# Kernel tuning notes

Hardware: AMD Instinct MI355X
Metric: run time of the kernel (lower is better)

## Reference

```python
import jax, jax.numpy as jnp
import numpy as np

B, S, HID = 2, 2048, 2048
NH, NOPE, ROPE = 16, 128, 64
HD = NOPE + ROPE          # 192
VHD = 128
KVR, QR = 512, 1536
FFN = 5632
THETA = 10000.0
EPS = 1e-6


def rmsnorm(x, w, eps=EPS):
    xf = x.astype(jnp.float32)
    rms = jnp.sqrt(jnp.mean(xf * xf, axis=-1, keepdims=True) + eps)
    return (xf / rms).astype(x.dtype) * w


def apply_rope(x, cos, sin):
    # x: (..., rope_dim); half-split rotation convention
    half = x.shape[-1] // 2
    x1, x2 = x[..., :half], x[..., half:]
    return jnp.concatenate([x1 * cos - x2 * sin, x2 * cos + x1 * sin], axis=-1)


def rope_tables(seq_len, dim, theta=THETA):
    inv_freq = 1.0 / (theta ** (jnp.arange(0, dim, 2, dtype=jnp.float32) / dim))
    t = jnp.arange(seq_len, dtype=jnp.float32)
    freqs = jnp.outer(t, inv_freq)           # (S, dim/2)
    return jnp.cos(freqs), jnp.sin(freqs)


def setup_inputs():
    key = jax.random.key(0)
    ks = jax.random.split(key, 10)
    def w(k, shape, fan_in):
        return jax.random.normal(k, shape, dtype=jnp.float32) * (fan_in ** -0.5)
    return {
        'x': jax.random.normal(ks[0], (B, S, HID), dtype=jnp.float32),
        'attn_norm_w': jnp.ones((HID,), jnp.float32),
        'wq_down': w(ks[1], (HID, QR), HID),
        'wq_up': w(ks[2], (QR, NH * HD), QR),
        'wkv_down': w(ks[3], (HID, KVR + ROPE), HID),
        'kv_norm_w': jnp.ones((KVR,), jnp.float32),
        'wkv_up': w(ks[4], (KVR, NH * (NOPE + VHD)), KVR),
        'wout': w(ks[5], (NH * VHD, HID), NH * VHD),
        'ffn_norm_w': jnp.ones((HID,), jnp.float32),
        'w_gate': w(ks[6], (HID, FFN), HID),
        'w_up': w(ks[7], (HID, FFN), HID),
        'w_down': w(ks[8], (FFN, HID), FFN),
    }


def reference(x, attn_norm_w, wq_down, wq_up, wkv_down, kv_norm_w, wkv_up, wout,
              ffn_norm_w, w_gate, w_up, w_down):
    scale = 1.0 / np.sqrt(HD)
    # --- attention sub-block ---
    h = rmsnorm(x, attn_norm_w)
    q = (h @ wq_down) @ wq_up                       # (B,S,NH*HD)
    q = q.reshape(B, S, NH, HD)
    q_nope, q_rope = q[..., :NOPE], q[..., NOPE:]
    kv_full = h @ wkv_down                          # (B,S,KVR+ROPE)
    kv_c, k_rope = kv_full[..., :KVR], kv_full[..., KVR:]
    kv_c = rmsnorm(kv_c, kv_norm_w)
    kv_exp = (kv_c @ wkv_up).reshape(B, S, NH, NOPE + VHD)
    k_nope, v = kv_exp[..., :NOPE], kv_exp[..., NOPE:]

    cos, sin = rope_tables(S, ROPE)                 # (S, ROPE/2)
    cos4, sin4 = cos[None, :, None, :], sin[None, :, None, :]
    q_rope = apply_rope(q_rope, cos4, sin4)         # (B,S,NH,ROPE)
    k_rope = apply_rope(k_rope[:, :, None, :], cos4, sin4)  # (B,S,1,ROPE)
    k_rope = jnp.broadcast_to(k_rope, (B, S, NH, ROPE))

    q_full = jnp.concatenate([q_nope, q_rope], axis=-1)     # (B,S,NH,HD)
    k = jnp.concatenate([k_nope, k_rope], axis=-1)          # (B,S,NH,HD)

    scores = jnp.einsum('bqhd,bkhd->bhqk', q_full, k) * scale
    causal = jnp.tril(jnp.ones((S, S), dtype=bool))
    scores = jnp.where(causal[None, None], scores, jnp.finfo(scores.dtype).min)
    probs = jax.nn.softmax(scores, axis=-1)
    attn = jnp.einsum('bhqk,bkhd->bqhd', probs, v).reshape(B, S, NH * VHD)
    x = x + attn @ wout

    # --- SwiGLU MLP sub-block ---
    h2 = rmsnorm(x, ffn_norm_w)
    ffn = (jax.nn.silu(h2 @ w_gate) * (h2 @ w_up)) @ w_down
    return x + ffn
```

## Files before the change

### kernel.cpp

```cpp
#include <hip/hip_runtime.h>
#include <hip/hip_bf16.h>


using bf16x8 = __attribute__((ext_vector_type(8))) short;
using f32x4  = __attribute__((ext_vector_type(4))) float;

#define GLOBAL_AS __attribute__((address_space(1)))
#define LDS_AS    __attribute__((address_space(3)))
#define MFMA16(a, b, c) __builtin_amdgcn_mfma_f32_16x16x32_bf16((a), (b), (c), 0, 0, 0)

static constexpr int Sc = 2048;

__device__ __forceinline__ void gload16(const void* g, void* l) {
  __builtin_amdgcn_global_load_lds((const GLOBAL_AS unsigned int*)g,
                                   (LDS_AS unsigned int*)l, 16, 0, 0);
}
__device__ __forceinline__ float bf2f(unsigned short u) {
  union { float f; unsigned int i; } x; x.i = ((unsigned int)u) << 16; return x.f;
}
__device__ __forceinline__ unsigned short f2bf(float f) {
  union { float f; unsigned int i; } x; x.f = f;
  unsigned int i = x.i;
  return (unsigned short)((i + 0x7fffu + ((i >> 16) & 1u)) >> 16);
}
__device__ __forceinline__ int swz4(int r) { return ((r >> 2) & 3) ^ (r & 3); }

__global__ void fill_k(float* out, float v, int n) {
  int i = blockIdx.x * 256 + threadIdx.x;
  if (i < n) out[i] = v;
}

__global__ __launch_bounds__(256) void wtrans(const float* __restrict__ W,
                                              unsigned short* __restrict__ WT,
                                              int K, int N) {
  __shared__ float t[64][65];
  const int n0 = blockIdx.x * 64, k0 = blockIdx.y * 64;
  const int tx = threadIdx.x & 15, ty = threadIdx.x >> 4;
#pragma unroll
  for (int i = 0; i < 4; ++i) {
    int k = k0 + ty + i * 16;
    const float4 v = *(const float4*)(W + (size_t)k * N + n0 + tx * 4);
    t[ty + i * 16][tx * 4 + 0] = v.x;
    t[ty + i * 16][tx * 4 + 1] = v.y;
    t[ty + i * 16][tx * 4 + 2] = v.z;
    t[ty + i * 16][tx * 4 + 3] = v.w;
  }
  __syncthreads();
  const int kx = threadIdx.x & 7, ny = threadIdx.x >> 3;
#pragma unroll
  for (int i = 0; i < 2; ++i) {
    int nl = ny + i * 32;
    unsigned short u[8];
#pragma unroll
    for (int j = 0; j < 8; ++j) u[j] = f2bf(t[kx * 8 + j][nl]);
    *(uint4*)(WT + (size_t)(n0 + nl) * K + k0 + kx * 8) = *(uint4*)u;
  }
}

__global__ void rope_tab(float* __restrict__ cosT, float* __restrict__ sinT) {
  int i = blockIdx.x * 256 + threadIdx.x;
  if (i >= Sc * 32) return;
  int s = i >> 5, j = i & 31;
  float inv = powf(10000.0f, -(float)j / 32.0f);
  float a = (float)s * inv;
  cosT[i] = cosf(a);
  sinT[i] = sinf(a);
}

__global__ __launch_bounds__(256) void rmsnorm_k(const float* __restrict__ in,
                                                 const float* __restrict__ w,
                                                 unsigned short* __restrict__ out,
                                                 int D, int istride, int ostride) {
  const int row = blockIdx.x;
  const float* x = in + (size_t)row * istride;
  float ss = 0.f;
  for (int c = threadIdx.x * 4; c < D; c += 1024) {
    const float4 v = *(const float4*)(x + c);
    ss += v.x * v.x + v.y * v.y + v.z * v.z + v.w * v.w;
  }
#pragma unroll
  for (int off = 1; off < 64; off <<= 1) ss += __shfl_xor(ss, off);
  __shared__ float part[4];
  if ((threadIdx.x & 63) == 0) part[threadIdx.x >> 6] = ss;
  __syncthreads();
  float tot = part[0] + part[1] + part[2] + part[3];
  float r = rsqrtf(tot / (float)D + 1e-6f);
  for (int c = threadIdx.x * 4; c < D; c += 1024) {
    const float4 v = *(const float4*)(x + c);
    ushort4 o;
    o.x = f2bf(v.x * r * w[c + 0]);
    o.y = f2bf(v.y * r * w[c + 1]);
    o.z = f2bf(v.z * r * w[c + 2]);
    o.w = f2bf(v.w * r * w[c + 3]);
    *(ushort4*)(out + (size_t)row * ostride + c) = o;
  }
}

enum { EPI_BF16 = 0, EPI_F32 = 1, EPI_ADDF32 = 2, EPI_SILU = 3 };

template <int EPI>
__global__ __launch_bounds__(256) void gemm_sb1(const unsigned short* __restrict__ A,
                                                const unsigned short* __restrict__ BT,
                                                void* __restrict__ Cp,
                                                const float* __restrict__ resid,
                                                const unsigned short* __restrict__ other,
                                                int M, int N, int K) {
  __shared__ unsigned short ldsA[128 * 64];
  __shared__ unsigned short ldsB[128 * 64];
  const int tid = threadIdx.x;
  const int w = tid >> 6, lane = tid & 63;
  const int rl = lane & 15, gh = lane >> 4;
  const int wm = (w >> 1) * 64, wn = (w & 1) * 64;

  const int nwg = gridDim.x;
  const int orig = blockIdx.x;
  const int qq = nwg >> 3, rr = nwg & 7;
  const int xcd = orig & 7, lidx = orig >> 3;
  const int fswz = (xcd < rr ? xcd * (qq + 1) : rr * (qq + 1) + (xcd - rr) * qq) + lidx;
  const int MT = M >> 7;
  const int m0 = (fswz % MT) * 128;
  const int n0 = (fswz / MT) * 128;

  const unsigned short* sA[4];
  const unsigned short* sB[4];
#pragma unroll
  for (int i = 0; i < 4; ++i) {
    int G = i * 256 + tid, r = G >> 3, sl = (G & 7) ^ (r & 7);
    sA[i] = A + (size_t)(m0 + r) * K + sl * 8;
    sB[i] = BT + (size_t)(n0 + r) * K + sl * 8;
  }
  auto STAGE = [&](int kt) {
    const int ko = kt * 64;
#pragma unroll
    for (int i = 0; i < 4; ++i) {
      gload16(sA[i] + ko, &ldsA[(i * 256 + w * 64) * 8]);
      gload16(sB[i] + ko, &ldsB[(i * 256 + w * 64) * 8]);
    }
  };

  int aoff[4], boff[4];
#pragma unroll
  for (int i = 0; i < 4; ++i) {
    aoff[i] = (wm + i * 16 + rl) * 64;
    boff[i] = (wn + i * 16 + rl) * 64;
  }

  f32x4 acc[4][4] = {};
  const int nk = K >> 6;

  STAGE(0);
  asm volatile("s_waitcnt vmcnt(0)" ::: "memory");
  __builtin_amdgcn_s_barrier();

  for (int kt = 0; kt < nk; ++kt) {
    bf16x8 a[4][2], b[4][2];
#pragma unroll
    for (int i = 0; i < 4; ++i)
#pragma unroll
      for (int ks = 0; ks < 2; ++ks) {
        const int ra = wm + i * 16 + rl;
        a[i][ks] = *(const bf16x8*)&ldsA[aoff[i] + ((((ks << 2) + gh)) ^ (ra & 7)) * 8];
        const int rb = wn + i * 16 + rl;
        b[i][ks] = *(const bf16x8*)&ldsB[boff[i] + ((((ks << 2) + gh)) ^ (rb & 7)) * 8];
      }
    asm volatile("s_waitcnt lgkmcnt(0)" ::: "memory");
    __builtin_amdgcn_sched_barrier(0);
    __builtin_amdgcn_s_setprio(1);
#pragma unroll
    for (int i = 0; i < 4; ++i)
#pragma unroll
      for (int j = 0; j < 4; ++j) acc[i][j] = MFMA16(a[i][0], b[j][0], acc[i][j]);
    __builtin_amdgcn_s_setprio(0);
    __builtin_amdgcn_sched_barrier(0);
    __builtin_amdgcn_s_barrier();
    STAGE((kt + 1 < nk) ? kt + 1 : nk - 1);
    __builtin_amdgcn_sched_barrier(0);
    __builtin_amdgcn_s_setprio(1);
#pragma unroll
    for (int i = 0; i < 4; ++i)
#pragma unroll
      for (int j = 0; j < 4; ++j) acc[i][j] = MFMA16(a[i][1], b[j][1], acc[i][j]);
    __builtin_amdgcn_s_setprio(0);
    __builtin_amdgcn_sched_barrier(0);
    asm volatile("s_waitcnt vmcnt(0)" ::: "memory");
    __builtin_amdgcn_s_barrier();
  }

#pragma unroll
  for (int i = 0; i < 4; ++i) {
#pragma unroll
    for (int j = 0; j < 4; ++j) {
#pragma unroll
      for (int rg = 0; rg < 4; ++rg) {
        const int row = m0 + wm + i * 16 + gh * 4 + rg;
        const int col = n0 + wn + j * 16 + rl;
        const size_t idx = (size_t)row * N + col;
        const float v = acc[i][j][rg];
        if constexpr (EPI == EPI_BF16) {
          ((unsigned short*)Cp)[idx] = f2bf(v);
        } else if constexpr (EPI == EPI_F32) {
          ((float*)Cp)[idx] = v;
        } else if constexpr (EPI == EPI_ADDF32) {
          ((float*)Cp)[idx] = v + resid[idx];
        } else {
          float gv = bf2f(other[idx]);
          float sg = gv / (1.f + __expf(-gv));
          ((unsigned short*)Cp)[idx] = f2bf(sg * v);
        }
      }
    }
  }
}

template <int EPI>
__global__ __launch_bounds__(256) void gemm_bt(const unsigned short* __restrict__ A,
                                               const unsigned short* __restrict__ BT,
                                               void* __restrict__ Cp,
                                               const float* __restrict__ resid,
                                               const unsigned short* __restrict__ other,
                                               int M, int N, int K) {
  __shared__ unsigned short ldsA[2][128 * 32];
  __shared__ unsigned short ldsB[2][128 * 32];
  const int tid = threadIdx.x;
  const int w = tid >> 6, lane = tid & 63;
  const int nwg = gridDim.x;
  const int orig = blockIdx.x;
  const int qq = nwg >> 3, rr = nwg & 7;
  const int xcd = orig & 7, lidx = orig >> 3;
  const int fswz = (xcd < rr ? xcd * (qq + 1) : rr * (qq + 1) + (xcd - rr) * qq) + lidx;
  const int m0 = (fswz & 31) * 128;
  const int n0 = (fswz >> 5) * 128;

  const int wm = (w >> 1) * 64, wn = (w & 1) * 64;
  const int rl = lane & 15, gsel = lane >> 4;

  const int p0 = w * 64 + lane;
  const int p1 = p0 + 256;
  const int r0 = p0 >> 2, r1 = p1 >> 2;
  const int g0 = (p0 & 3) ^ swz4(r0), g1 = (p1 & 3) ^ swz4(r1);
  const unsigned short* gA0 = A + (size_t)(m0 + r0) * K + g0 * 8;
  const unsigned short* gA1 = A + (size_t)(m0 + r1) * K + g1 * 8;
  const unsigned short* gB0 = BT + (size_t)(n0 + r0) * K + g0 * 8;
  const unsigned short* gB1 = BT + (size_t)(n0 + r1) * K + g1 * 8;
  const int dA0 = (w * 64) * 8, dA1 = dA0 + 2048;

  int aoff[4], boff[4];
#pragma unroll
  for (int i = 0; i < 4; ++i) {
    int ra = wm + i * 16 + rl;
    aoff[i] = ra * 32 + (gsel ^ swz4(ra)) * 8;
    int rb = wn + i * 16 + rl;
    boff[i] = rb * 32 + (gsel ^ swz4(rb)) * 8;
  }

  auto STAGE = [&](int kt, int p) {
    const int ko = kt * 32;
    gload16(gA0 + ko, &ldsA[p][dA0]);
    gload16(gA1 + ko, &ldsA[p][dA1]);
    gload16(gB0 + ko, &ldsB[p][dA0]);
    gload16(gB1 + ko, &ldsB[p][dA1]);
  };

  f32x4 acc[4][4] = {};
  const int nk = K >> 5;

  STAGE(0, 0);
  STAGE(1, 1);
  for (int kt = 0; kt < nk; ++kt) {
    asm volatile("s_waitcnt vmcnt(4)" ::: "memory");
    __builtin_amdgcn_s_barrier();
    __builtin_amdgcn_sched_barrier(0);
    const unsigned short* lA = &ldsA[kt & 1][0];
    const unsigned short* lB = &ldsB[kt & 1][0];
    bf16x8 a[4], b[4];
#pragma unroll
    for (int i = 0; i < 4; ++i) a[i] = *(const bf16x8*)&lA[aoff[i]];
#pragma unroll
    for (int i = 0; i < 4; ++i) b[i] = *(const bf16x8*)&lB[boff[i]];
    __builtin_amdgcn_s_setprio(1);
#pragma unroll
    for (int i = 0; i < 4; ++i)
#pragma unroll
      for (int j = 0; j < 4; ++j) acc[i][j] = MFMA16(a[i], b[j], acc[i][j]);
    __builtin_amdgcn_s_setprio(0);
    __builtin_amdgcn_sched_barrier(0);
    __builtin_amdgcn_s_barrier();
    const int nxt = (kt + 2 < nk) ? kt + 2 : nk - 1;
    STAGE(nxt, kt & 1);
  }

#pragma unroll
  for (int i = 0; i < 4; ++i) {
#pragma unroll
    for (int j = 0; j < 4; ++j) {
#pragma unroll
      for (int rg = 0; rg < 4; ++rg) {
        const int row = m0 + wm + i * 16 + gsel * 4 + rg;
        const int col = n0 + wn + j * 16 + rl;
        const size_t idx = (size_t)row * N + col;
        const float v = acc[i][j][rg];
        if constexpr (EPI == EPI_BF16) {
          ((unsigned short*)Cp)[idx] = f2bf(v);
        } else if constexpr (EPI == EPI_F32) {
          ((float*)Cp)[idx] = v;
        } else if constexpr (EPI == EPI_ADDF32) {
          ((float*)Cp)[idx] = v + resid[idx];
        } else {
          float gv = bf2f(other[idx]);
          float sg = gv / (1.f + __expf(-gv));
          ((unsigned short*)Cp)[idx] = f2bf(sg * v);
        }
      }
    }
  }
}

__global__ __launch_bounds__(256) void repack_q(const unsigned short* __restrict__ q,
                                                const float* __restrict__ cosT,
                                                const float* __restrict__ sinT,
                                                unsigned short* __restrict__ Qc) {
  const int row = blockIdx.x;
  const int b = row >> 11, s = row & 2047;
  const float scale = 0.07216878364870322f;
  const unsigned short* qr = q + (size_t)row * 3072;
  for (int i = threadIdx.x; i < 3072; i += 256) {
    int h = i / 192, d = i - h * 192;
    float v;
    if (d < 128) {
      v = bf2f(qr[h * 192 + d]);
    } else {
      int j = d - 128;
      int jj = j & 31;
      float x1 = bf2f(qr[h * 192 + 128 + jj]);
      float x2 = bf2f(qr[h * 192 + 160 + jj]);
      float c = cosT[s * 32 + jj], sn = sinT[s * 32 + jj];
      v = (j < 32) ? (x1 * c - x2 * sn) : (x2 * c + x1 * sn);
    }
    Qc[((size_t)(b * 16 + h) * Sc + s) * 192 + d] = f2bf(v * scale);
  }
}

__global__ __launch_bounds__(256) void repack_kv(const unsigned short* __restrict__ kvex,
                                                 const float* __restrict__ kvf,
                                                 const float* __restrict__ cosT,
                                                 const float* __restrict__ sinT,
                                                 unsigned short* __restrict__ Kc,
                                                 unsigned short* __restrict__ VT) {
  __shared__ unsigned short vt_lds[32][136];
  const int bid = blockIdx.x;
  const int st = bid & 63;
  const int h = (bid >> 6) & 15;
  const int b = bid >> 10;
  const int s0 = st * 32;
  const int tid = threadIdx.x;
  const size_t KcBase = (size_t)(b * 16 + h) * Sc;
  for (int i = tid; i < 32 * 32; i += 256) {
    int r = i >> 5, g = i & 31;
    uint4 vdat = *(const uint4*)(kvex + (size_t)(b * Sc + s0 + r) * 4096 + h * 256 + g * 8);
    if (g < 16) {
      *(uint4*)(Kc + (KcBase + s0 + r) * 192 + g * 8) = vdat;
    } else {
      *(uint4*)(&vt_lds[r][(g - 16) * 8]) = vdat;
    }
  }
  for (int i = tid; i < 32 * 64; i += 256) {
    int r = i >> 6, d = i & 63;
    int s = s0 + r;
    int jj = d & 31;
    const float* kvrow = kvf + (size_t)(b * Sc + s) * 640;
    float x1 = kvrow[512 + jj], x2 = kvrow[544 + jj];
    float c = cosT[s * 32 + jj], sn = sinT[s * 32 + jj];
    float v = (d < 32) ? (x1 * c - x2 * sn) : (x2 * c + x1 * sn);
    Kc[(KcBase + s) * 192 + 128 + d] = f2bf(v);
  }
  __syncthreads();
  const int f = tid >> 1, sh = (tid & 1) * 16;
  unsigned int vals[8];
#pragma unroll
  for (int k2 = 0; k2 < 8; ++k2) {
    unsigned int lo = vt_lds[sh + 2 * k2][f];
    unsigned int hi = vt_lds[sh + 2 * k2 + 1][f];
    vals[k2] = lo | (hi << 16);
  }
  unsigned short* dst = VT + ((size_t)(b * 16 + h) * 128 + f) * Sc + s0 + sh;
  ((uint4*)dst)[0] = make_uint4(vals[0], vals[1], vals[2], vals[3]);
  ((uint4*)dst)[1] = make_uint4(vals[4], vals[5], vals[6], vals[7]);
}

__global__ __launch_bounds__(512) void attn_k(const unsigned short* __restrict__ Qc,
                                              const unsigned short* __restrict__ Kc,
                                              const unsigned short* __restrict__ VT,
                                              unsigned short* __restrict__ Ob) {
  __shared__ unsigned short lds_k[2][64 * 192];
  __shared__ unsigned short lds_v[2][128 * 64];
  __shared__ __align__(16) unsigned short p_lds[8][16 * 72];
  const int tid = threadIdx.x, w = tid >> 6, lane = tid & 63;
  const int rl = lane & 15, gh = lane >> 4;
  const int bidx = blockIdx.x;
  const int bh = bidx & 31;
  const int qt = 15 - (bidx >> 5);
  const unsigned short* Qh = Qc + (size_t)bh * Sc * 192;
  const unsigned short* Kh = Kc + (size_t)bh * Sc * 192;
  const unsigned short* Vh = VT + (size_t)bh * 128 * Sc;
  const int qr0 = qt * 128 + w * 16;

  bf16x8 qf[6];
#pragma unroll
  for (int kk = 0; kk < 6; ++kk)
    qf[kk] = *(const bf16x8*)(Qh + (size_t)(qr0 + rl) * 192 + kk * 32 + gh * 8);

  f32x4 o[8] = {};
  float mrun[4] = {-1e30f, -1e30f, -1e30f, -1e30f};
  float srun[4] = {0.f, 0.f, 0.f, 0.f};

  int kr[3], kg[3];
#pragma unroll
  for (int j = 0; j < 3; ++j) {
    int G = j * 512 + tid;
    int r = G / 24, gq = G - r * 24;
    kr[j] = r;
    kg[j] = (gq & ~7) | ((gq & 7) ^ (r & 7));
  }
  int vr[2], vg[2];
#pragma unroll
  for (int j = 0; j < 2; ++j) {
    int G = j * 512 + tid;
    int r = G >> 3;
    vr[j] = r;
    vg[j] = (G & 7) ^ (r & 7);
  }

  auto STAGE = [&](int t, int b) {
    const int k0 = t * 64;
#pragma unroll
    for (int j = 0; j < 3; ++j)
      gload16(Kh + (size_t)(k0 + kr[j]) * 192 + kg[j] * 8,
              &lds_k[b][(j * 512 + w * 64) * 8]);
#pragma unroll
    for (int j = 0; j < 2; ++j)
      gload16(Vh + (size_t)vr[j] * Sc + k0 + vg[j] * 8,
              &lds_v[b][(j * 512 + w * 64) * 8]);
  };

  STAGE(0, 0);
  asm volatile("s_waitcnt vmcnt(0)" ::: "memory");
  __builtin_amdgcn_s_barrier();
  __builtin_amdgcn_sched_barrier(0);

  const int nt = 2 * qt + 2;
  int cur = 0;
  for (int t = 0; t < nt; ++t) {
    if (t + 1 < nt) STAGE(t + 1, cur ^ 1);
    const int k0 = t * 64;
    if (k0 <= qr0 + 15) {
      const unsigned short* lk = lds_k[cur];
      const unsigned short* lv = lds_v[cur];
      f32x4 s[4] = {};
      __builtin_amdgcn_s_setprio(1);
#pragma unroll
      for (int kk = 0; kk < 6; ++kk) {
        const int gq = kk * 4 + gh;
#pragma unroll
        for (int ks = 0; ks < 4; ++ks) {
          const int krow = ks * 16 + rl;
          const int ph = (gq & ~7) | ((gq & 7) ^ (krow & 7));
          bf16x8 kf = *(const bf16x8*)&lk[krow * 192 + ph * 8];
          s[ks] = MFMA16(qf[kk], kf, s[ks]);
        }
      }
      __builtin_amdgcn_s_setprio(0);
      if (k0 + 63 > qr0) {
#pragma unroll
        for (int ks = 0; ks < 4; ++ks)
#pragma unroll
          for (int rg = 0; rg < 4; ++rg) {
            int qrow = qr0 + gh * 4 + rg;
            if (k0 + ks * 16 + rl > qrow) s[ks][rg] = -1e30f;
          }
      }
      float tmax[4];
#pragma unroll
      for (int rg = 0; rg < 4; ++rg) {
        float v = fmaxf(fmaxf(s[0][rg], s[1][rg]), fmaxf(s[2][rg], s[3][rg]));
        v = fmaxf(v, __shfl_xor(v, 1));
        v = fmaxf(v, __shfl_xor(v, 2));
        v = fmaxf(v, __shfl_xor(v, 4));
        v = fmaxf(v, __shfl_xor(v, 8));
        tmax[rg] = v;
      }
      int need = !(tmax[0] <= mrun[0] + 8.f && tmax[1] <= mrun[1] + 8.f &&
                   tmax[2] <= mrun[2] + 8.f && tmax[3] <= mrun[3] + 8.f);
      if (__any(need)) {
        float al[4];
#pragma unroll
        for (int rg = 0; rg < 4; ++rg) {
          float mn = fmaxf(mrun[rg], tmax[rg]);
          al[rg] = __expf(mrun[rg] - mn);
          mrun[rg] = mn;
          srun[rg] *= al[rg];
        }
#pragma unroll
        for (int i = 0; i < 8; ++i)
#pragma unroll
          for (int rg = 0; rg < 4; ++rg) o[i][rg] *= al[rg];
      }
      unsigned short* pw = p_lds[w];
#pragma unroll
      for (int ks = 0; ks < 4; ++ks)
#pragma unroll
        for (int rg = 0; rg < 4; ++rg) {
          float p = __expf(s[ks][rg] - mrun[rg]);
          srun[rg] += p;
          pw[(gh * 4 + rg) * 72 + ks * 16 + rl] = f2bf(p);
        }
      bf16x8 pa0 = *(const bf16x8*)&pw[rl * 72 + 0 * 32 + gh * 8];
      bf16x8 pa1 = *(const bf16x8*)&pw[rl * 72 + 1 * 32 + gh * 8];
      __builtin_amdgcn_s_setprio(1);
#pragma unroll
      for (int vf = 0; vf < 8; ++vf) {
        const int row = vf * 16 + rl;
        bf16x8 v0 = *(const bf16x8*)&lv[row * 64 + ((0 * 4 + gh) ^ (row & 7)) * 8];
        o[vf] = MFMA16(pa0, v0, o[vf]);
        bf16x8 v1 = *(const bf16x8*)&lv[row * 64 + ((1 * 4 + gh) ^ (row & 7)) * 8];
        o[vf] = MFMA16(pa1, v1, o[vf]);
      }
      __builtin_amdgcn_s_setprio(0);
    }
    asm volatile("s_waitcnt vmcnt(0)" ::: "memory");
    __builtin_amdgcn_s_barrier();
    __builtin_amdgcn_sched_barrier(0);
    cur ^= 1;
  }
  float rd[4];
#pragma unroll
  for (int rg = 0; rg < 4; ++rg) {
    float rs = srun[rg];
    rs += __shfl_xor(rs, 1);
    rs += __shfl_xor(rs, 2);
    rs += __shfl_xor(rs, 4);
    rs += __shfl_xor(rs, 8);
    rd[rg] = 1.f / rs;
  }
  const int b = bh >> 4, hh = bh & 15;
#pragma unroll
  for (int vf = 0; vf < 8; ++vf) {
#pragma unroll
    for (int rg = 0; rg < 4; ++rg) {
      int srow = qr0 + gh * 4 + rg;
      int col = hh * 128 + vf * 16 + rl;
      Ob[((size_t)(b * Sc) + srow) * 2048 + col] = f2bf(o[vf][rg] * rd[rg]);
    }
  }
}

extern "C" void kernel_launch(void* const* d_in, const int* in_sizes, int n_in,
                              void* d_out, int out_size, void* d_ws, size_t ws_size,
                              hipStream_t stream) {
  (void)in_sizes; (void)n_in;
  const float* x    = (const float*)d_in[0];
  const float* anw  = (const float*)d_in[1];
  const float* wqd  = (const float*)d_in[2];
  const float* wqu  = (const float*)d_in[3];
  const float* wkvd = (const float*)d_in[4];
  const float* kvnw = (const float*)d_in[5];
  const float* wkvu = (const float*)d_in[6];
  const float* wout = (const float*)d_in[7];
  const float* fnw  = (const float*)d_in[8];
  const float* wg   = (const float*)d_in[9];
  const float* wu   = (const float*)d_in[10];
  const float* wd   = (const float*)d_in[11];
  float* out = (float*)d_out;

  char* ws = (char*)d_ws;
  size_t off = 0;
  auto alloc = [&](size_t bytes) -> char* {
    char* p = ws + off;
    off += (bytes + 255) & ~(size_t)255;
    return p;
  };
  unsigned short* wslot = (unsigned short*)alloc(5632ull * 2048 * 2);
  float* cosT           = (float*)alloc(2048ull * 32 * 4);
  float* sinT           = (float*)alloc(2048ull * 32 * 4);
  unsigned short* hbuf  = (unsigned short*)alloc(4096ull * 2048 * 2);
  char* arena           = alloc(4096ull * 1536 * 2 + 4096ull * 3072 * 2);
  float* kvf            = (float*)alloc(4096ull * 640 * 4);
  unsigned short* kvn   = (unsigned short*)alloc(4096ull * 512 * 2);
  unsigned short* Qc    = (unsigned short*)alloc(32ull * 2048 * 192 * 2);
  unsigned short* Kc    = (unsigned short*)alloc(32ull * 2048 * 192 * 2);
  unsigned short* VTb   = (unsigned short*)alloc(32ull * 128 * 2048 * 2);
  const size_t NEED = off;

  if (ws_size < NEED) {
    fill_k<<<dim3((out_size + 255) / 256), dim3(256), 0, stream>>>(
        out, (float)(ws_size >> 20), out_size);
    return;
  }

  unsigned short* qd    = (unsigned short*)arena;
  unsigned short* q     = (unsigned short*)(arena + 4096ull * 1536 * 2);
  unsigned short* kvex  = (unsigned short*)arena;
  unsigned short* h     = hbuf;
  unsigned short* attnb = hbuf;
  unsigned short* h2    = hbuf;
  unsigned short* gbuf  = Qc;
  float* x2             = out;

  dim3 blk(256), blk512(512);
  rope_tab<<<dim3(256), blk, 0, stream>>>(cosT, sinT);
  rmsnorm_k<<<dim3(4096), blk, 0, stream>>>(x, anw, h, 2048, 2048, 2048);

  wtrans<<<dim3(24, 32), blk, 0, stream>>>(wqd, wslot, 2048, 1536);
  gemm_sb1<EPI_BF16><<<dim3(32 * 12), blk, 0, stream>>>(h, wslot, qd, nullptr, nullptr, 4096, 1536, 2048);
  wtrans<<<dim3(48, 24), blk, 0, stream>>>(wqu, wslot, 1536, 3072);
  gemm_sb1<EPI_BF16><<<dim3(32 * 24), blk, 0, stream>>>(qd, wslot, q, nullptr, nullptr, 4096, 3072, 1536);
  repack_q<<<dim3(4096), blk, 0, stream>>>(q, cosT, sinT, Qc);

  wtrans<<<dim3(9, 32), blk, 0, stream>>>(wkvd, wslot, 2048, 576);
  gemm_bt<EPI_F32><<<dim3(5 * 32), blk, 0, stream>>>(h, wslot, kvf, nullptr, nullptr, 4096, 640, 2048);
  rmsnorm_k<<<dim3(4096), blk, 0, stream>>>(kvf, kvnw, kvn, 512, 640, 512);
  wtrans<<<dim3(64, 8), blk, 0, stream>>>(wkvu, wslot, 512, 4096);
  gemm_sb1<EPI_BF16><<<dim3(32 * 32), blk, 0, stream>>>(kvn, wslot, kvex, nullptr, nullptr, 4096, 4096, 512);
  repack_kv<<<dim3(2048), blk, 0, stream>>>(kvex, kvf, cosT, sinT, Kc, VTb);

  attn_k<<<dim3(512), blk512, 0, stream>>>(Qc, Kc, VTb, attnb);
  wtrans<<<dim3(32, 32), blk, 0, stream>>>(wout, wslot, 2048, 2048);
  gemm_sb1<EPI_ADDF32><<<dim3(32 * 16), blk, 0, stream>>>(attnb, wslot, x2, x, nullptr, 4096, 2048, 2048);

  rmsnorm_k<<<dim3(4096), blk, 0, stream>>>(x2, fnw, h2, 2048, 2048, 2048);
  wtrans<<<dim3(88, 32), blk, 0, stream>>>(wg, wslot, 2048, 5632);
  gemm_sb1<EPI_BF16><<<dim3(32 * 44), blk, 0, stream>>>(h2, wslot, gbuf, nullptr, nullptr, 4096, 5632, 2048);
  wtrans<<<dim3(88, 32), blk, 0, stream>>>(wu, wslot, 2048, 5632);
  gemm_sb1<EPI_SILU><<<dim3(32 * 44), blk, 0, stream>>>(h2, wslot, gbuf, nullptr, gbuf, 4096, 5632, 2048);
  wtrans<<<dim3(32, 88), blk, 0, stream>>>(wd, wslot, 5632, 2048);
  gemm_sb1<EPI_ADDF32><<<dim3(32 * 16), blk, 0, stream>>>(gbuf, wslot, out, x2, nullptr, 4096, 2048, 5632);
}
```

Measured before the change: 769.7 us.

## Replace GEMMs with 512-thread 128x256 tile kernel using single-buffered BK=64 staging

```diff
diff --git a/kernel.cpp b/kernel.cpp
--- a/kernel.cpp
+++ b/kernel.cpp
@@ -213,80 +213,96 @@
 }
 
 template <int EPI>
-__global__ __launch_bounds__(256) void gemm_bt(const unsigned short* __restrict__ A,
-                                               const unsigned short* __restrict__ BT,
-                                               void* __restrict__ Cp,
-                                               const float* __restrict__ resid,
-                                               const unsigned short* __restrict__ other,
-                                               int M, int N, int K) {
-  __shared__ unsigned short ldsA[2][128 * 32];
-  __shared__ unsigned short ldsB[2][128 * 32];
+__global__ __launch_bounds__(512) void gemm_sb2(const unsigned short* __restrict__ A,
+                                                const unsigned short* __restrict__ BT,
+                                                void* __restrict__ Cp,
+                                                const float* __restrict__ resid,
+                                                const unsigned short* __restrict__ other,
+                                                int M, int N, int K) {
+  __shared__ unsigned short ldsA[128 * 64];
+  __shared__ unsigned short ldsB[256 * 64];
   const int tid = threadIdx.x;
   const int w = tid >> 6, lane = tid & 63;
+  const int rl = lane & 15, gh = lane >> 4;
+  const int wm = (w >> 2) * 64, wn = (w & 3) * 64;
+
   const int nwg = gridDim.x;
   const int orig = blockIdx.x;
   const int qq = nwg >> 3, rr = nwg & 7;
   const int xcd = orig & 7, lidx = orig >> 3;
   const int fswz = (xcd < rr ? xcd * (qq + 1) : rr * (qq + 1) + (xcd - rr) * qq) + lidx;
-  const int m0 = (fswz & 31) * 128;
-  const int n0 = (fswz >> 5) * 128;
-
-  const int wm = (w >> 1) * 64, wn = (w & 1) * 64;
-  const int rl = lane & 15, gsel = lane >> 4;
-
-  const int p0 = w * 64 + lane;
-  const int p1 = p0 + 256;
-  const int r0 = p0 >> 2, r1 = p1 >> 2;
-  const int g0 = (p0 & 3) ^ swz4(r0), g1 = (p1 & 3) ^ swz4(r1);
-  const unsigned short* gA0 = A + (size_t)(m0 + r0) * K + g0 * 8;
-  const unsigned short* gA1 = A + (size_t)(m0 + r1) * K + g1 * 8;
-  const unsigned short* gB0 = BT + (size_t)(n0 + r0) * K + g0 * 8;
-  const unsigned short* gB1 = BT + (size_t)(n0 + r1) * K + g1 * 8;
-  const int dA0 = (w * 64) * 8, dA1 = dA0 + 2048;
+  const int MT = M >> 7;
+  const int m0 = (fswz % MT) * 128;
+  const int n0 = (fswz / MT) * 256;
+
+  const unsigned short* sA[2];
+#pragma unroll
+  for (int i = 0; i < 2; ++i) {
+    int G = i * 512 + tid, r = G >> 3, sl = (G & 7) ^ (r & 7);
+    sA[i] = A + (size_t)(m0 + r) * K + sl * 8;
+  }
+  const unsigned short* sB[4];
+#pragma unroll
+  for (int i = 0; i < 4; ++i) {
+    int G = i * 512 + tid, r = G >> 3, sl = (G & 7) ^ (r & 7);
+    sB[i] = BT + (size_t)(n0 + r) * K + sl * 8;
+  }
+  auto STAGE = [&](int kt) {
+    const int ko = kt * 64;
+#pragma unroll
+    for (int i = 0; i < 2; ++i)
+      gload16(sA[i] + ko, &ldsA[(i * 512 + w * 64) * 8]);
+#pragma unroll
+    for (int i = 0; i < 4; ++i)
+      gload16(sB[i] + ko, &ldsB[(i * 512 + w * 64) * 8]);
+  };
 
   int aoff[4], boff[4];
 #pragma unroll
   for (int i = 0; i < 4; ++i) {
-    int ra = wm + i * 16 + rl;
-    aoff[i] = ra * 32 + (gsel ^ swz4(ra)) * 8;
-    int rb = wn + i * 16 + rl;
-    boff[i] = rb * 32 + (gsel ^ swz4(rb)) * 8;
-  }
-
-  auto STAGE = [&](int kt, int p) {
-    const int ko = kt * 32;
-    gload16(gA0 + ko, &ldsA[p][dA0]);
-    gload16(gA1 + ko, &ldsA[p][dA1]);
-    gload16(gB0 + ko, &ldsB[p][dA0]);
-    gload16(gB1 + ko, &ldsB[p][dA1]);
-  };
+    aoff[i] = (wm + i * 16 + rl) * 64;
+    boff[i] = (wn + i * 16 + rl) * 64;
+  }
 
   f32x4 acc[4][4] = {};
-  const int nk = K >> 5;
-
-  STAGE(0, 0);
-  STAGE(1, 1);
+  const int nk = K >> 6;
+
+  STAGE(0);
+  asm volatile("s_waitcnt vmcnt(0)" ::: "memory");
+  __builtin_amdgcn_s_barrier();
+
   for (int kt = 0; kt < nk; ++kt) {
-    asm volatile("s_waitcnt vmcnt(4)" ::: "memory");
+    bf16x8 a[4][2], b[4][2];
+#pragma unroll
+    for (int i = 0; i < 4; ++i)
+#pragma unroll
+      for (int ks = 0; ks < 2; ++ks) {
+        const int ra = wm + i * 16 + rl;
+        a[i][ks] = *(const bf16x8*)&ldsA[aoff[i] + ((((ks << 2) + gh)) ^ (ra & 7)) * 8];
+        const int rb = wn + i * 16 + rl;
+        b[i][ks] = *(const bf16x8*)&ldsB[boff[i] + ((((ks << 2) + gh)) ^ (rb & 7)) * 8];
+      }
+    asm volatile("s_waitcnt lgkmcnt(0)" ::: "memory");
+    __builtin_amdgcn_sched_barrier(0);
+    __builtin_amdgcn_s_setprio(1);
+#pragma unroll
+    for (int i = 0; i < 4; ++i)
+#pragma unroll
+      for (int j = 0; j < 4; ++j) acc[i][j] = MFMA16(a[i][0], b[j][0], acc[i][j]);
+    __builtin_amdgcn_s_setprio(0);
+    __builtin_amdgcn_sched_barrier(0);
     __builtin_amdgcn_s_barrier();
-    __builtin_amdgcn_sched_barrier(0);
-    const unsigned short* lA = &ldsA[kt & 1][0];
-    const unsigned short* lB = &ldsB[kt & 1][0];
-    bf16x8 a[4], b[4];
-#pragma unroll
-    for (int i = 0; i < 4; ++i) a[i] = *(const bf16x8*)&lA[aoff[i]];
-#pragma unroll
-    for (int i = 0; i < 4; ++i) b[i] = *(const bf16x8*)&lB[boff[i]];
+    STAGE((kt + 1 < nk) ? kt + 1 : nk - 1);
+    __builtin_amdgcn_sched_barrier(0);
     __builtin_amdgcn_s_setprio(1);
 #pragma unroll
     for (int i = 0; i < 4; ++i)
 #pragma unroll
-      for (int j = 0; j < 4; ++j) acc[i][j] = MFMA16(a[i], b[j], acc[i][j]);
+      for (int j = 0; j < 4; ++j) acc[i][j] = MFMA16(a[i][1], b[j][1], acc[i][j]);
     __builtin_amdgcn_s_setprio(0);
     __builtin_amdgcn_sched_barrier(0);
+    asm volatile("s_waitcnt vmcnt(0)" ::: "memory");
     __builtin_amdgcn_s_barrier();
-    const int nxt = (kt + 2 < nk) ? kt + 2 : nk - 1;
-    STAGE(nxt, kt & 1);
   }
 
 #pragma unroll
@@ -295,7 +311,7 @@
     for (int j = 0; j < 4; ++j) {
 #pragma unroll
       for (int rg = 0; rg < 4; ++rg) {
-        const int row = m0 + wm + i * 16 + gsel * 4 + rg;
+        const int row = m0 + wm + i * 16 + gh * 4 + rg;
         const int col = n0 + wn + j * 16 + rl;
         const size_t idx = (size_t)row * N + col;
         const float v = acc[i][j][rg];
@@ -610,27 +626,27 @@
   rmsnorm_k<<<dim3(4096), blk, 0, stream>>>(x, anw, h, 2048, 2048, 2048);
 
   wtrans<<<dim3(24, 32), blk, 0, stream>>>(wqd, wslot, 2048, 1536);
-  gemm_sb1<EPI_BF16><<<dim3(32 * 12), blk, 0, stream>>>(h, wslot, qd, nullptr, nullptr, 4096, 1536, 2048);
+  gemm_sb2<EPI_BF16><<<dim3(32 * 6), blk512, 0, stream>>>(h, wslot, qd, nullptr, nullptr, 4096, 1536, 2048);
   wtrans<<<dim3(48, 24), blk, 0, stream>>>(wqu, wslot, 1536, 3072);
-  gemm_sb1<EPI_BF16><<<dim3(32 * 24), blk, 0, stream>>>(qd, wslot, q, nullptr, nullptr, 4096, 3072, 1536);
+  gemm_sb2<EPI_BF16><<<dim3(32 * 12), blk512, 0, stream>>>(qd, wslot, q, nullptr, nullptr, 4096, 3072, 1536);
   repack_q<<<dim3(4096), blk, 0, stream>>>(q, cosT, sinT, Qc);
 
   wtrans<<<dim3(9, 32), blk, 0, stream>>>(wkvd, wslot, 2048, 576);
-  gemm_bt<EPI_F32><<<dim3(5 * 32), blk, 0, stream>>>(h, wslot, kvf, nullptr, nullptr, 4096, 640, 2048);
+  gemm_sb1<EPI_F32><<<dim3(32 * 5), blk, 0, stream>>>(h, wslot, kvf, nullptr, nullptr, 4096, 640, 2048);
   rmsnorm_k<<<dim3(4096), blk, 0, stream>>>(kvf, kvnw, kvn, 512, 640, 512);
   wtrans<<<dim3(64, 8), blk, 0, stream>>>(wkvu, wslot, 512, 4096);
-  gemm_sb1<EPI_BF16><<<dim3(32 * 32), blk, 0, stream>>>(kvn, wslot, kvex, nullptr, nullptr, 4096, 4096, 512);
+  gemm_sb2<EPI_BF16><<<dim3(32 * 16), blk512, 0, stream>>>(kvn, wslot, kvex, nullptr, nullptr, 4096, 4096, 512);
   repack_kv<<<dim3(2048), blk, 0, stream>>>(kvex, kvf, cosT, sinT, Kc, VTb);
 
   attn_k<<<dim3(512), blk512, 0, stream>>>(Qc, Kc, VTb, attnb);
   wtrans<<<dim3(32, 32), blk, 0, stream>>>(wout, wslot, 2048, 2048);
-  gemm_sb1<EPI_ADDF32><<<dim3(32 * 16), blk, 0, stream>>>(attnb, wslot, x2, x, nullptr, 4096, 2048, 2048);
+  gemm_sb2<EPI_ADDF32><<<dim3(32 * 8), blk512, 0, stream>>>(attnb, wslot, x2, x, nullptr, 4096, 2048, 2048);
 
   rmsnorm_k<<<dim3(4096), blk, 0, stream>>>(x2, fnw, h2, 2048, 2048, 2048);
   wtrans<<<dim3(88, 32), blk, 0, stream>>>(wg, wslot, 2048, 5632);
-  gemm_sb1<EPI_BF16><<<dim3(32 * 44), blk, 0, stream>>>(h2, wslot, gbuf, nullptr, nullptr, 4096, 5632, 2048);
+  gemm_sb2<EPI_BF16><<<dim3(32 * 22), blk512, 0, stream>>>(h2, wslot, gbuf, nullptr, nullptr, 4096, 5632, 2048);
   wtrans<<<dim3(88, 32), blk, 0, stream>>>(wu, wslot, 2048, 5632);
-  gemm_sb1<EPI_SILU><<<dim3(32 * 44), blk, 0, stream>>>(h2, wslot, gbuf, nullptr, gbuf, 4096, 5632, 2048);
+  gemm_sb2<EPI_SILU><<<dim3(32 * 22), blk512, 0, stream>>>(h2, wslot, gbuf, nullptr, gbuf, 4096, 5632, 2048);
   wtrans<<<dim3(32, 88), blk, 0, stream>>>(wd, wslot, 5632, 2048);
-  gemm_sb1<EPI_ADDF32><<<dim3(32 * 16), blk, 0, stream>>>(gbuf, wslot, out, x2, nullptr, 4096, 2048, 5632);
-}
+  gemm_sb2<EPI_ADDF32><<<dim3(32 * 8), blk512, 0, stream>>>(gbuf, wslot, out, x2, nullptr, 4096, 2048, 5632);
+}
```

Result: slower. 846.5 us (+10.0%).

## Single-buffer K tile in attention to cut LDS and route kv-down GEMM to gemm_sb1

Applied to the files above, without the earlier changes.

```diff
diff --git a/kernel.cpp b/kernel.cpp
--- a/kernel.cpp
+++ b/kernel.cpp
@@ -193,109 +193,6 @@
 #pragma unroll
       for (int rg = 0; rg < 4; ++rg) {
         const int row = m0 + wm + i * 16 + gh * 4 + rg;
-        const int col = n0 + wn + j * 16 + rl;
-        const size_t idx = (size_t)row * N + col;
-        const float v = acc[i][j][rg];
-        if constexpr (EPI == EPI_BF16) {
-          ((unsigned short*)Cp)[idx] = f2bf(v);
-        } else if constexpr (EPI == EPI_F32) {
-          ((float*)Cp)[idx] = v;
-        } else if constexpr (EPI == EPI_ADDF32) {
-          ((float*)Cp)[idx] = v + resid[idx];
-        } else {
-          float gv = bf2f(other[idx]);
-          float sg = gv / (1.f + __expf(-gv));
-          ((unsigned short*)Cp)[idx] = f2bf(sg * v);
-        }
-      }
-    }
-  }
-}
-
-template <int EPI>
-__global__ __launch_bounds__(256) void gemm_bt(const unsigned short* __restrict__ A,
-                                               const unsigned short* __restrict__ BT,
-                                               void* __restrict__ Cp,
-                                               const float* __restrict__ resid,
-                                               const unsigned short* __restrict__ other,
-                                               int M, int N, int K) {
-  __shared__ unsigned short ldsA[2][128 * 32];
-  __shared__ unsigned short ldsB[2][128 * 32];
-  const int tid = threadIdx.x;
-  const int w = tid >> 6, lane = tid & 63;
-  const int nwg = gridDim.x;
-  const int orig = blockIdx.x;
-  const int qq = nwg >> 3, rr = nwg & 7;
-  const int xcd = orig & 7, lidx = orig >> 3;
-  const int fswz = (xcd < rr ? xcd * (qq + 1) : rr * (qq + 1) + (xcd - rr) * qq) + lidx;
-  const int m0 = (fswz & 31) * 128;
-  const int n0 = (fswz >> 5) * 128;
-
-  const int wm = (w >> 1) * 64, wn = (w & 1) * 64;
-  const int rl = lane & 15, gsel = lane >> 4;
-
-  const int p0 = w * 64 + lane;
-  const int p1 = p0 + 256;
-  const int r0 = p0 >> 2, r1 = p1 >> 2;
-  const int g0 = (p0 & 3) ^ swz4(r0), g1 = (p1 & 3) ^ swz4(r1);
-  const unsigned short* gA0 = A + (size_t)(m0 + r0) * K + g0 * 8;
-  const unsigned short* gA1 = A + (size_t)(m0 + r1) * K + g1 * 8;
-  const unsigned short* gB0 = BT + (size_t)(n0 + r0) * K + g0 * 8;
-  const unsigned short* gB1 = BT + (size_t)(n0 + r1) * K + g1 * 8;
-  const int dA0 = (w * 64) * 8, dA1 = dA0 + 2048;
-
-  int aoff[4], boff[4];
-#pragma unroll
-  for (int i = 0; i < 4; ++i) {
-    int ra = wm + i * 16 + rl;
-    aoff[i] = ra * 32 + (gsel ^ swz4(ra)) * 8;
-    int rb = wn + i * 16 + rl;
-    boff[i] = rb * 32 + (gsel ^ swz4(rb)) * 8;
-  }
-
-  auto STAGE = [&](int kt, int p) {
-    const int ko = kt * 32;
-    gload16(gA0 + ko, &ldsA[p][dA0]);
-    gload16(gA1 + ko, &ldsA[p][dA1]);
-    gload16(gB0 + ko, &ldsB[p][dA0]);
-    gload16(gB1 + ko, &ldsB[p][dA1]);
-  };
-
-  f32x4 acc[4][4] = {};
-  const int nk = K >> 5;
-
-  STAGE(0, 0);
-  STAGE(1, 1);
-  for (int kt = 0; kt < nk; ++kt) {
-    asm volatile("s_waitcnt vmcnt(4)" ::: "memory");
-    __builtin_amdgcn_s_barrier();
-    __builtin_amdgcn_sched_barrier(0);
-    const unsigned short* lA = &ldsA[kt & 1][0];
-    const unsigned short* lB = &ldsB[kt & 1][0];
-    bf16x8 a[4], b[4];
-#pragma unroll
-    for (int i = 0; i < 4; ++i) a[i] = *(const bf16x8*)&lA[aoff[i]];
-#pragma unroll
-    for (int i = 0; i < 4; ++i) b[i] = *(const bf16x8*)&lB[boff[i]];
-    __builtin_amdgcn_s_setprio(1);
-#pragma unroll
-    for (int i = 0; i < 4; ++i)
-#pragma unroll
-      for (int j = 0; j < 4; ++j) acc[i][j] = MFMA16(a[i], b[j], acc[i][j]);
-    __builtin_amdgcn_s_setprio(0);
-    __builtin_amdgcn_sched_barrier(0);
-    __builtin_amdgcn_s_barrier();
-    const int nxt = (kt + 2 < nk) ? kt + 2 : nk - 1;
-    STAGE(nxt, kt & 1);
-  }
-
-#pragma unroll
-  for (int i = 0; i < 4; ++i) {
-#pragma unroll
-    for (int j = 0; j < 4; ++j) {
-#pragma unroll
-      for (int rg = 0; rg < 4; ++rg) {
-        const int row = m0 + wm + i * 16 + gsel * 4 + rg;
         const int col = n0 + wn + j * 16 + rl;
         const size_t idx = (size_t)row * N + col;
         const float v = acc[i][j][rg];
@@ -391,7 +288,7 @@
                                               const unsigned short* __restrict__ Kc,
                                               const unsigned short* __restrict__ VT,
                                               unsigned short* __restrict__ Ob) {
-  __shared__ unsigned short lds_k[2][64 * 192];
+  __shared__ unsigned short lds_k[64 * 192];
   __shared__ unsigned short lds_v[2][128 * 64];
   __shared__ __align__(16) unsigned short p_lds[8][16 * 72];
   const int tid = threadIdx.x, w = tid >> 6, lane = tid & 63;
@@ -430,32 +327,35 @@
     vg[j] = (G & 7) ^ (r & 7);
   }
 
-  auto STAGE = [&](int t, int b) {
+  auto STAGE_K = [&](int t) {
     const int k0 = t * 64;
 #pragma unroll
     for (int j = 0; j < 3; ++j)
       gload16(Kh + (size_t)(k0 + kr[j]) * 192 + kg[j] * 8,
-              &lds_k[b][(j * 512 + w * 64) * 8]);
+              &lds_k[(j * 512 + w * 64) * 8]);
+  };
+  auto STAGE_V = [&](int t, int b) {
+    const int k0 = t * 64;
 #pragma unroll
     for (int j = 0; j < 2; ++j)
       gload16(Vh + (size_t)vr[j] * Sc + k0 + vg[j] * 8,
               &lds_v[b][(j * 512 + w * 64) * 8]);
   };
 
-  STAGE(0, 0);
+  STAGE_K(0);
+  STAGE_V(0, 0);
   asm volatile("s_waitcnt vmcnt(0)" ::: "memory");
   __builtin_amdgcn_s_barrier();
   __builtin_amdgcn_sched_barrier(0);
 
   const int nt = 2 * qt + 2;
-  int cur = 0;
+  int vcur = 0;
   for (int t = 0; t < nt; ++t) {
-    if (t + 1 < nt) STAGE(t + 1, cur ^ 1);
+    if (t + 1 < nt) STAGE_V(t + 1, vcur ^ 1);
     const int k0 = t * 64;
-    if (k0 <= qr0 + 15) {
-      const unsigned short* lk = lds_k[cur];
-      const unsigned short* lv = lds_v[cur];
-      f32x4 s[4] = {};
+    const bool docomp = (k0 <= qr0 + 15);
+    f32x4 s[4] = {};
+    if (docomp) {
       __builtin_amdgcn_s_setprio(1);
 #pragma unroll
       for (int kk = 0; kk < 6; ++kk) {
@@ -464,11 +364,18 @@
         for (int ks = 0; ks < 4; ++ks) {
           const int krow = ks * 16 + rl;
           const int ph = (gq & ~7) | ((gq & 7) ^ (krow & 7));
-          bf16x8 kf = *(const bf16x8*)&lk[krow * 192 + ph * 8];
+          bf16x8 kf = *(const bf16x8*)&lds_k[krow * 192 + ph * 8];
           s[ks] = MFMA16(qf[kk], kf, s[ks]);
         }
       }
       __builtin_amdgcn_s_setprio(0);
+      asm volatile("s_waitcnt lgkmcnt(0)" ::: "memory");
+    }
+    __builtin_amdgcn_sched_barrier(0);
+    __builtin_amdgcn_s_barrier();
+    if (t + 1 < nt) STAGE_K(t + 1);
+    __builtin_amdgcn_sched_barrier(0);
+    if (docomp) {
       if (k0 + 63 > qr0) {
 #pragma unroll
         for (int ks = 0; ks < 4; ++ks)
@@ -515,6 +422,7 @@
         }
       bf16x8 pa0 = *(const bf16x8*)&pw[rl * 72 + 0 * 32 + gh * 8];
       bf16x8 pa1 = *(const bf16x8*)&pw[rl * 72 + 1 * 32 + gh * 8];
+      const unsigned short* lv = lds_v[vcur];
       __builtin_amdgcn_s_setprio(1);
 #pragma unroll
       for (int vf = 0; vf < 8; ++vf) {
@@ -529,7 +437,7 @@
     asm volatile("s_waitcnt vmcnt(0)" ::: "memory");
     __builtin_amdgcn_s_barrier();
     __builtin_amdgcn_sched_barrier(0);
-    cur ^= 1;
+    vcur ^= 1;
   }
   float rd[4];
 #pragma unroll
@@ -616,7 +524,7 @@
   repack_q<<<dim3(4096), blk, 0, stream>>>(q, cosT, sinT, Qc);
 
   wtrans<<<dim3(9, 32), blk, 0, stream>>>(wkvd, wslot, 2048, 576);
-  gemm_bt<EPI_F32><<<dim3(5 * 32), blk, 0, stream>>>(h, wslot, kvf, nullptr, nullptr, 4096, 640, 2048);
+  gemm_sb1<EPI_F32><<<dim3(32 * 5), blk, 0, stream>>>(h, wslot, kvf, nullptr, nullptr, 4096, 640, 2048);
   rmsnorm_k<<<dim3(4096), blk, 0, stream>>>(kvf, kvnw, kvn, 512, 640, 512);
   wtrans<<<dim3(64, 8), blk, 0, stream>>>(wkvu, wslot, 512, 4096);
   gemm_sb1<EPI_BF16><<<dim3(32 * 32), blk, 0, stream>>>(kvn, wslot, kvex, nullptr, nullptr, 4096, 4096, 512);
```

After: 756.4 us. Within noise of the previous version (-1.7%).
